# Optimization experiments

Measured on AMD Instinct MI355X. Metric: run time of the kernel, lower is better.

The kernel has to match this reference:

```python
import jax, jax.numpy as jnp
import numpy as np

N_IN = 128 * 128   # flattened stimulus frame
N0 = 4096          # layer 0 neurons
N1 = 1024          # layer 1 neurons
T = 600            # timesteps
MAX_DELAY = 16
DECAY = 0.9
THRESH = 1.0
V_RESET = 0.0


def setup_inputs() -> dict:
    key = jax.random.key(0)
    k1, k2, k3, k4 = jax.random.split(key, 4)
    stim = jax.random.uniform(k1, (128, 128, T), dtype=jnp.float32) * 20.0
    W0 = jax.random.normal(k2, (N0, N_IN), dtype=jnp.float32) * 0.02
    W1 = jax.random.normal(k3, (N1, N0), dtype=jnp.float32) * 0.05
    delays = jax.random.randint(k4, (N1, N0), 0, MAX_DELAY, dtype=jnp.int32)
    return {"stim": stim, "W0": W0, "W1": W1, "delays": delays}


def reference(stim, W0, W1, delays):
    # stim: [H, W, T]; flatten frames -> [T, N_IN]
    t_len = stim.shape[2]
    x = stim.reshape(-1, t_len).T
    jpre = jnp.arange(W0.shape[0])  # presynaptic index per column of W1

    def lif(v, I, dtype):
        v = v * DECAY + I
        s = (v >= THRESH).astype(dtype)
        v = jnp.where(s > 0, V_RESET, v)
        return v, s

    def step(carry, xt):
        v0, v1, buf = carry
        # synapse 0: dense weighted sum of input frame
        I0 = W0 @ xt                                  # [N0]
        v0, s0 = lif(v0, I0, xt.dtype)
        # push newest spikes into circular delay buffer [MAX_DELAY, N0]
        buf = jnp.concatenate([s0[None, :], buf[:-1]], axis=0)
        # synapse 1: per-connection delayed spike gather
        delayed = buf[delays, jpre[None, :]]          # [N1, N0]
        I1 = jnp.sum(W1 * delayed, axis=1)            # [N1]
        v1, s1 = lif(v1, I1, xt.dtype)
        return (v0, v1, buf), (s0, s1)

    init = (
        jnp.zeros((W0.shape[0],), stim.dtype),
        jnp.zeros((W1.shape[0],), stim.dtype),
        jnp.zeros((MAX_DELAY, W0.shape[0]), stim.dtype),
    )
    # loop runs for t in [1, T) as in the original feedforward
    _, (S0, S1) = jax.lax.scan(step, init, x[1:])
    # spike_times layout: [n_neurons, T-1]
    return S0.T, S1.T
```

## Files before the change

kernel.cpp:

```cpp
#include <hip/hip_runtime.h>
#include <stdint.h>
#include <math.h>

#define T_STEPS 599
#define T_RAW   600
#define NIN     16384
#define N0      4096
#define N1      1024
#define S0W     24
#define TAUP    640

typedef double d4 __attribute__((ext_vector_type(4)));

static const size_t OFF_I0T = 0;
static const size_t SZ_I0T  = (size_t)T_STEPS * N0 * 4;
static const size_t OFF_S0B = OFF_I0T + SZ_I0T;
static const size_t SZ_S0B  = (size_t)N0 * S0W * 4;
static const size_t OFF_XT  = OFF_S0B + SZ_S0B;
static const size_t SZ_XT   = (size_t)TAUP * NIN * 4;

__global__ __launch_bounds__(256) void transpose_stim(const float* __restrict__ stim,
                                                      float* __restrict__ Xt) {
    __shared__ float T[64][65];
    const int tau0 = blockIdx.x * 64;
    const int k0   = blockIdx.y * 64;
    const int tid  = threadIdx.x;
    const int kk = tid >> 2;
    const int tb = tid & 3;
#pragma unroll
    for (int q = 0; q < 16; ++q) {
        const int tl = tb + 4 * q;
        const int tg = tau0 + tl;
        float v = 0.0f;
        if (tg <= T_STEPS - 1) v = stim[(size_t)(k0 + kk) * T_RAW + tg + 1];
        T[kk][tl] = v;
    }
    __syncthreads();
    const int tt = tid >> 2;
    const int kq = (tid & 3) * 16;
#pragma unroll
    for (int j = 0; j < 4; ++j) {
        const int kl = kq + 4 * j;
        float4 o;
        o.x = T[kl + 0][tt]; o.y = T[kl + 1][tt];
        o.z = T[kl + 2][tt]; o.w = T[kl + 3][tt];
        *reinterpret_cast<float4*>(&Xt[(size_t)(tau0 + tt) * NIN + k0 + kl]) = o;
    }
}

__global__ __launch_bounds__(256, 5) void gemm_i0_xt(const float* __restrict__ W0,
                                                     const float* __restrict__ Xt,
                                                     float* __restrict__ I0T) {
    __shared__ __align__(16) char smem[31744];
    float* As0 = (float*)(smem);
    float* As1 = (float*)(smem + 4608);
    float* Bt0 = (float*)(smem + 9216);
    float* Bt1 = (float*)(smem + 20480);
    const int tid  = threadIdx.x;
    const int lane = tid & 63;
    const int wid  = tid >> 6;
    const int kbase = 16 * (wid >> 1);
    const int coff  = 32 * (wid & 1);
    const int flat = blockIdx.x;
    const int idx  = (flat & 7) * 160 + (flat >> 3);
    const int n0   = (idx / 10) * 32;
    const int tau0 = (idx % 10) * 64;
    const int r15  = lane & 15;
    const int c    = lane >> 4;

    d4 zero = {0.0, 0.0, 0.0, 0.0};
    const double ap1 = (c == 0) ? 1.0 : 0.0;
    const double bp1 = (c == 0) ? (double)r15 : 0.0;
    d4 pcol = __builtin_amdgcn_mfma_f64_16x16x4f64(ap1, bp1, zero, 0, 0, 0);
    const double ap2 = (c == 0) ? (double)r15 : 0.0;
    const double bp2 = (c == 0) ? 1.0 : 0.0;
    d4 prow = __builtin_amdgcn_mfma_f64_16x16x4f64(ap2, bp2, zero, 0, 0, 0);
    int rowr[4], colr[4];
#pragma unroll
    for (int r = 0; r < 4; ++r) {
        int cc = (int)pcol[r]; cc = cc < 0 ? 0 : (cc > 15 ? 15 : cc);
        int rw = (int)prow[r]; rw = rw < 0 ? 0 : (rw > 15 ? 15 : rw);
        colr[r] = cc; rowr[r] = rw;
    }

    const int ar   = tid >> 3;
    const int ac4  = (tid & 7) * 4;
    const int btau = tid >> 2;
    const int bk8  = (tid & 3) * 8;

    const float* aP  = W0 + (size_t)(n0 + ar) * NIN + ac4;
    const float* xP  = Xt + (size_t)(tau0 + btau) * NIN + bk8;

    float4 aR, bR0, bR1;

#define XLOAD()                                                           \
    aR  = *reinterpret_cast<const float4*>(aP);                           \
    bR0 = *reinterpret_cast<const float4*>(xP);                           \
    bR1 = *reinterpret_cast<const float4*>(xP + 4);                       \
    aP += 32; xP += 32;

#define XSTAGE(AS, BS)                                                    \
    *reinterpret_cast<float4*>(&AS[ar * 36 + ac4]) = aR;                  \
    *reinterpret_cast<float4*>(&BS[btau * 44 + bk8]) = bR0;               \
    *reinterpret_cast<float4*>(&BS[btau * 44 + bk8 + 4]) = bR1;

    d4 c00 = {0,0,0,0}, c01 = {0,0,0,0};
    d4 c10 = {0,0,0,0}, c11 = {0,0,0,0};

#define XMFMA(AS, BS)                                                     \
    {                                                                     \
        __builtin_amdgcn_s_setprio(1);                                    \
        const float4 a0f = *reinterpret_cast<const float4*>(&AS[r15 * 36 + kbase + 4 * c]);        \
        const float4 a1f = *reinterpret_cast<const float4*>(&AS[(16 + r15) * 36 + kbase + 4 * c]); \
        const float4 b0f = *reinterpret_cast<const float4*>(&BS[(coff + r15) * 44 + kbase + 4 * c]);      \
        const float4 b1f = *reinterpret_cast<const float4*>(&BS[(coff + 16 + r15) * 44 + kbase + 4 * c]); \
        c00 = __builtin_amdgcn_mfma_f64_16x16x4f64((double)a0f.x, (double)b0f.x, c00, 0, 0, 0);    \
        c01 = __builtin_amdgcn_mfma_f64_16x16x4f64((double)a0f.x, (double)b1f.x, c01, 0, 0, 0);    \
        c10 = __builtin_amdgcn_mfma_f64_16x16x4f64((double)a1f.x, (double)b0f.x, c10, 0, 0, 0);    \
        c11 = __builtin_amdgcn_mfma_f64_16x16x4f64((double)a1f.x, (double)b1f.x, c11, 0, 0, 0);    \
        c00 = __builtin_amdgcn_mfma_f64_16x16x4f64((double)a0f.y, (double)b0f.y, c00, 0, 0, 0);    \
        c01 = __builtin_amdgcn_mfma_f64_16x16x4f64((double)a0f.y, (double)b1f.y, c01, 0, 0, 0);    \
        c10 = __builtin_amdgcn_mfma_f64_16x16x4f64((double)a1f.y, (double)b0f.y, c10, 0, 0, 0);    \
        c11 = __builtin_amdgcn_mfma_f64_16x16x4f64((double)a1f.y, (double)b1f.y, c11, 0, 0, 0);    \
        c00 = __builtin_amdgcn_mfma_f64_16x16x4f64((double)a0f.z, (double)b0f.z, c00, 0, 0, 0);    \
        c01 = __builtin_amdgcn_mfma_f64_16x16x4f64((double)a0f.z, (double)b1f.z, c01, 0, 0, 0);    \
        c10 = __builtin_amdgcn_mfma_f64_16x16x4f64((double)a1f.z, (double)b0f.z, c10, 0, 0, 0);    \
        c11 = __builtin_amdgcn_mfma_f64_16x16x4f64((double)a1f.z, (double)b1f.z, c11, 0, 0, 0);    \
        c00 = __builtin_amdgcn_mfma_f64_16x16x4f64((double)a0f.w, (double)b0f.w, c00, 0, 0, 0);    \
        c01 = __builtin_amdgcn_mfma_f64_16x16x4f64((double)a0f.w, (double)b1f.w, c01, 0, 0, 0);    \
        c10 = __builtin_amdgcn_mfma_f64_16x16x4f64((double)a1f.w, (double)b0f.w, c10, 0, 0, 0);    \
        c11 = __builtin_amdgcn_mfma_f64_16x16x4f64((double)a1f.w, (double)b1f.w, c11, 0, 0, 0);    \
        __builtin_amdgcn_s_setprio(0);                                    \
    }

    XLOAD();
    for (int chp = 0; chp < 256; ++chp) {
        XSTAGE(As0, Bt0);
        __syncthreads();
        XLOAD();
        XMFMA(As0, Bt0);
        XSTAGE(As1, Bt1);
        __syncthreads();
        if (chp + 1 < 256) { XLOAD(); }
        XMFMA(As1, Bt1);
    }
#undef XLOAD
#undef XSTAGE
#undef XMFMA

    __syncthreads();
    double* Cred = (double*)smem;

#define CRED_OP(OP)                                                       \
    _Pragma("unroll")                                                     \
    for (int r = 0; r < 4; ++r) {                                         \
        const int ro = rowr[r], co = coff + colr[r];                      \
        Cred[(co     ) * 32 + ro     ] OP c00[r];                         \
        Cred[(co + 16) * 32 + ro     ] OP c01[r];                         \
        Cred[(co     ) * 32 + ro + 16] OP c10[r];                         \
        Cred[(co + 16) * 32 + ro + 16] OP c11[r];                         \
    }
    if (wid < 2)  { CRED_OP(=) }
    __syncthreads();
    if (wid >= 2) { CRED_OP(+=) }
    __syncthreads();
#undef CRED_OP

    const int scol = tid >> 2;
    const int srow = (tid & 3) * 8;
    const int tcol = tau0 + scol;
    if (tcol < T_STEPS) {
        const double* cp = &Cred[scol * 32 + srow];
        float4 o0, o1;
        o0.x = (float)cp[0]; o0.y = (float)cp[1]; o0.z = (float)cp[2]; o0.w = (float)cp[3];
        o1.x = (float)cp[4]; o1.y = (float)cp[5]; o1.z = (float)cp[6]; o1.w = (float)cp[7];
        float* op = &I0T[(size_t)tcol * N0 + n0 + srow];
        *reinterpret_cast<float4*>(op)     = o0;
        *reinterpret_cast<float4*>(op + 4) = o1;
    }
}

__global__ __launch_bounds__(256, 5) void gemm_i0_fb(const float* __restrict__ W0,
                                                     const float* __restrict__ stim,
                                                     float* __restrict__ I0T) {
    __shared__ __align__(16) char smem[27904];
    float* As0 = (float*)(smem);
    float* As1 = (float*)(smem + 4736);
    float* Bs0 = (float*)(smem + 9472);
    float* Bs1 = (float*)(smem + 18688);
    const int tid  = threadIdx.x;
    const int lane = tid & 63;
    const int wid  = tid >> 6;
    const int kbase = 16 * (wid >> 1);
    const int coff  = 32 * (wid & 1);
    const int flat = blockIdx.x;
    const int idx  = (flat & 7) * 160 + (flat >> 3);
    const int n0   = (idx / 10) * 32;
    const int tau0 = (idx % 10) * 64;
    const int r15  = lane & 15;
    const int c    = lane >> 4;
    d4 zero = {0.0, 0.0, 0.0, 0.0};
    const double ap1 = (c == 0) ? 1.0 : 0.0;
    const double bp1 = (c == 0) ? (double)r15 : 0.0;
    d4 pcol = __builtin_amdgcn_mfma_f64_16x16x4f64(ap1, bp1, zero, 0, 0, 0);
    const double ap2 = (c == 0) ? (double)r15 : 0.0;
    const double bp2 = (c == 0) ? 1.0 : 0.0;
    d4 prow = __builtin_amdgcn_mfma_f64_16x16x4f64(ap2, bp2, zero, 0, 0, 0);
    int rowr[4], colr[4];
#pragma unroll
    for (int r = 0; r < 4; ++r) {
        int cc = (int)pcol[r]; cc = cc < 0 ? 0 : (cc > 15 ? 15 : cc);
        int rw = (int)prow[r]; rw = rw < 0 ? 0 : (rw > 15 ? 15 : rw);
        colr[r] = cc; rowr[r] = rw;
    }
    const int ar  = tid >> 3;
    const int ac4 = (tid & 7) * 4;
    const int br  = tid >> 4;
    const int bc4 = (tid & 15) * 4;
    const int t0g = tau0 + bc4;
    const bool fastB = (tau0 + 68) <= T_RAW;
    const float* aP  = W0 + (size_t)(n0 + ar) * NIN + ac4;
    const float* bP0 = stim + (size_t)br * T_RAW + t0g;
    const float* bP1 = stim + (size_t)(br + 16) * T_RAW + t0g;
    float4 aR, bRa, bRb;
#define FLOAD()                                                           \
    aR = *reinterpret_cast<const float4*>(aP);                            \
    if (fastB) {                                                          \
        float4 f0 = *reinterpret_cast<const float4*>(bP0);                \
        float  e0 = bP0[4];                                               \
        bRa.x = f0.y; bRa.y = f0.z; bRa.z = f0.w; bRa.w = e0;             \
        float4 f1 = *reinterpret_cast<const float4*>(bP1);                \
        float  e1 = bP1[4];                                               \
        bRb.x = f1.y; bRb.y = f1.z; bRb.z = f1.w; bRb.w = e1;             \
    } else {                                                              \
        bRa.x = (t0g + 0 < T_STEPS) ? bP0[1] : 0.0f;                      \
        bRa.y = (t0g + 1 < T_STEPS) ? bP0[2] : 0.0f;                      \
        bRa.z = (t0g + 2 < T_STEPS) ? bP0[3] : 0.0f;                      \
        bRa.w = (t0g + 3 < T_STEPS) ? bP0[4] : 0.0f;                      \
        bRb.x = (t0g + 0 < T_STEPS) ? bP1[1] : 0.0f;                      \
        bRb.y = (t0g + 1 < T_STEPS) ? bP1[2] : 0.0f;                      \
        bRb.z = (t0g + 2 < T_STEPS) ? bP1[3] : 0.0f;                      \
        bRb.w = (t0g + 3 < T_STEPS) ? bP1[4] : 0.0f;                      \
    }                                                                     \
    aP += 32; bP0 += 32 * T_RAW; bP1 += 32 * T_RAW;
#define FSTAGE(AS, BS)                                                    \
    *reinterpret_cast<float4*>(&AS[ar * 37 + ac4]) = aR;                  \
    *reinterpret_cast<float4*>(&BS[br * 72 + bc4]) = bRa;                 \
    *reinterpret_cast<float4*>(&BS[(br + 16) * 72 + bc4]) = bRb;
#define FKSTEP(AS, BS, KK)                                                \
    {                                                                     \
        const double a0 = (double)AS[r15 * 37 + (KK)];                    \
        const double a1 = (double)AS[(16 + r15) * 37 + (KK)];             \
        const double b0 = (double)BS[(KK) * 72 + coff + r15];             \
        const double b1 = (double)BS[(KK) * 72 + coff + 16 + r15];        \
        c00 = __builtin_amdgcn_mfma_f64_16x16x4f64(a0, b0, c00, 0, 0, 0); \
        c01 = __builtin_amdgcn_mfma_f64_16x16x4f64(a0, b1, c01, 0, 0, 0); \
        c10 = __builtin_amdgcn_mfma_f64_16x16x4f64(a1, b0, c10, 0, 0, 0); \
        c11 = __builtin_amdgcn_mfma_f64_16x16x4f64(a1, b1, c11, 0, 0, 0); \
    }
#define FMFMA(AS, BS)                                                     \
    __builtin_amdgcn_s_setprio(1);                                        \
    FKSTEP(AS, BS, kbase + c);                                            \
    FKSTEP(AS, BS, kbase + 4 + c);                                        \
    FKSTEP(AS, BS, kbase + 8 + c);                                        \
    FKSTEP(AS, BS, kbase + 12 + c);                                       \
    __builtin_amdgcn_s_setprio(0);
    d4 c00 = {0,0,0,0}, c01 = {0,0,0,0};
    d4 c10 = {0,0,0,0}, c11 = {0,0,0,0};
    FLOAD();
    for (int chp = 0; chp < 256; ++chp) {
        FSTAGE(As0, Bs0);
        __syncthreads();
        FLOAD();
        FMFMA(As0, Bs0);
        FSTAGE(As1, Bs1);
        __syncthreads();
        if (chp + 1 < 256) { FLOAD(); }
        FMFMA(As1, Bs1);
    }
#undef FLOAD
#undef FSTAGE
#undef FKSTEP
#undef FMFMA
    __syncthreads();
    double* Cred = (double*)smem;
#define CRED_OP(OP)                                                       \
    _Pragma("unroll")                                                     \
    for (int r = 0; r < 4; ++r) {                                         \
        const int ro = rowr[r], co = coff + colr[r];                      \
        Cred[(co     ) * 32 + ro     ] OP c00[r];                         \
        Cred[(co + 16) * 32 + ro     ] OP c01[r];                         \
        Cred[(co     ) * 32 + ro + 16] OP c10[r];                         \
        Cred[(co + 16) * 32 + ro + 16] OP c11[r];                         \
    }
    if (wid < 2)  { CRED_OP(=) }
    __syncthreads();
    if (wid >= 2) { CRED_OP(+=) }
    __syncthreads();
#undef CRED_OP
    const int scol = tid >> 2;
    const int srow = (tid & 3) * 8;
    const int tcol = tau0 + scol;
    if (tcol < T_STEPS) {
        const double* cp = &Cred[scol * 32 + srow];
        float4 o0, o1;
        o0.x = (float)cp[0]; o0.y = (float)cp[1]; o0.z = (float)cp[2]; o0.w = (float)cp[3];
        o1.x = (float)cp[4]; o1.y = (float)cp[5]; o1.z = (float)cp[6]; o1.w = (float)cp[7];
        float* op = &I0T[(size_t)tcol * N0 + n0 + srow];
        *reinterpret_cast<float4*>(op)     = o0;
        *reinterpret_cast<float4*>(op + 4) = o1;
    }
}

__global__ void lif0(const float* __restrict__ I0T, uint32_t* __restrict__ S0P) {
#pragma clang fp contract(off)
    const int n = blockIdx.x * 64 + threadIdx.x;
    uint32_t* rowp = S0P + n * S0W;
    rowp[0] = 0u;
    rowp[20] = 0u; rowp[21] = 0u; rowp[22] = 0u; rowp[23] = 0u;
    float v = 0.0f;
    uint32_t word = 0;
    int t = 0;
    for (; t + 8 <= T_STEPS; t += 8) {
        float I[8];
#pragma unroll
        for (int u = 0; u < 8; ++u) I[u] = I0T[(size_t)(t + u) * N0 + n];
#pragma unroll
        for (int u = 0; u < 8; ++u) {
            const int tt = t + u;
            float a = v * 0.9f;
            v = a + I[u];
            if (v >= 1.0f) { word |= (1u << (tt & 31)); v = 0.0f; }
            if ((tt & 31) == 31) { rowp[1 + (tt >> 5)] = word; word = 0; }
        }
    }
    for (; t < T_STEPS; ++t) {
        float I = I0T[(size_t)t * N0 + n];
        float a = v * 0.9f;
        v = a + I;
        if (v >= 1.0f) { word |= (1u << (t & 31)); v = 0.0f; }
        if ((t & 31) == 31) { rowp[1 + (t >> 5)] = word; word = 0; }
    }
    rowp[1 + (T_STEPS >> 5)] = word;
}

__global__ __launch_bounds__(128) void gather_lif1(const float* __restrict__ W1,
                                                   const int* __restrict__ delays,
                                                   const uint32_t* __restrict__ S0P,
                                                   float* __restrict__ out) {
#pragma clang fp contract(off)
    __shared__ double  wl[N0];
    __shared__ uint8_t dl[N0];
    __shared__ float   i1row[T_RAW];
    const int j   = blockIdx.x;
    const int tid = threadIdx.x;
    for (int q = tid; q < N0 / 4; q += 128) {
        const float4 w4 = *reinterpret_cast<const float4*>(&W1[(size_t)j * N0 + 4 * q]);
        wl[4 * q + 0] = (double)w4.x; wl[4 * q + 1] = (double)w4.y;
        wl[4 * q + 2] = (double)w4.z; wl[4 * q + 3] = (double)w4.w;
        const int4 dv = *reinterpret_cast<const int4*>(&delays[(size_t)j * N0 + 4 * q]);
        dl[4 * q + 0] = (uint8_t)dv.x; dl[4 * q + 1] = (uint8_t)dv.y;
        dl[4 * q + 2] = (uint8_t)dv.z; dl[4 * q + 3] = (uint8_t)dv.w;
    }
    __syncthreads();
    const int t5 = 5 * tid;
    double a0 = 0.0, a1 = 0.0, a2 = 0.0, a3 = 0.0, a4 = 0.0;
    const uint32_t* rp0 = S0P + 1;
#pragma unroll 2
    for (int i = 0; i < N0; ++i) {
        const int s0  = t5 - (int)dl[i];
        const double w = wl[i];
        const int widx = (s0 >> 5);
        const int sh   = s0 & 31;
        const uint32_t lo = rp0[widx];
        const uint32_t hi = rp0[widx + 1];
        const uint32_t w5 = (uint32_t)(((((uint64_t)hi) << 32) | lo) >> sh);
        a0 = fma((double)( w5       & 1u), w, a0);
        a1 = fma((double)((w5 >> 1) & 1u), w, a1);
        a2 = fma((double)((w5 >> 2) & 1u), w, a2);
        a3 = fma((double)((w5 >> 3) & 1u), w, a3);
        a4 = fma((double)((w5 >> 4) & 1u), w, a4);
        rp0 += S0W;
    }
    if (tid < 120) {
        i1row[t5 + 0] = (float)a0;
        i1row[t5 + 1] = (float)a1;
        i1row[t5 + 2] = (float)a2;
        i1row[t5 + 3] = (float)a3;
        i1row[t5 + 4] = (float)a4;
    }
    __syncthreads();
    if (tid == 0) {
        float* o = out + (size_t)N0 * T_STEPS + (size_t)j * T_STEPS;
        float v = 0.0f;
        for (int t = 0; t < T_STEPS; ++t) {
            float a = v * 0.9f;
            v = a + i1row[t];
            float s = 0.0f;
            if (v >= 1.0f) { s = 1.0f; v = 0.0f; }
            o[t] = s;
        }
    }
}

__global__ void expand_out(const uint32_t* __restrict__ S0P,
                           float* __restrict__ out) {
    const int t = blockIdx.x * 256 + threadIdx.x;
    if (t >= T_STEPS) return;
    const int row = blockIdx.y;
    uint32_t b = (S0P[row * S0W + 1 + (t >> 5)] >> (t & 31)) & 1u;
    out[(size_t)row * T_STEPS + t] = (float)b;
}

extern "C" void kernel_launch(void* const* d_in, const int* in_sizes, int n_in,
                              void* d_out, int out_size, void* d_ws, size_t ws_size,
                              hipStream_t stream) {
    const float* stim   = (const float*)d_in[0];
    const float* W0     = (const float*)d_in[1];
    const float* W1     = (const float*)d_in[2];
    const int*   delays = (const int*)d_in[3];

    char* ws = (char*)d_ws;
    float*    I0T  = (float*)(ws + OFF_I0T);
    uint32_t* S0b  = (uint32_t*)(ws + OFF_S0B);
    float*    Xt   = (float*)(ws + OFF_XT);
    float*    out  = (float*)d_out;

    if (ws_size >= OFF_XT + SZ_XT) {
        hipLaunchKernelGGL(transpose_stim, dim3(10, 256), dim3(256), 0, stream, stim, Xt);
        hipLaunchKernelGGL(gemm_i0_xt,     dim3(1280),    dim3(256), 0, stream, W0, Xt, I0T);
    } else {
        hipLaunchKernelGGL(gemm_i0_fb,     dim3(1280),    dim3(256), 0, stream, W0, stim, I0T);
    }
    hipLaunchKernelGGL(lif0,        dim3(64),    dim3(64),  0, stream, I0T, S0b);
    hipLaunchKernelGGL(gather_lif1, dim3(1024),  dim3(128), 0, stream, W1, delays, S0b, out);
    hipLaunchKernelGGL(expand_out,  dim3(3, N0), dim3(256), 0, stream, S0b, out);
}
```

Baseline: 2.205 ms.

## Fuse S0 output expansion into lif0 and split gather across two halves

The layer-0 LIF kernel now writes float spikes to the output directly, going through a shared-memory transpose tile, so the separate expand_out kernel is removed. The delayed-gather kernel is split so each block handles half of the presynaptic neurons, which doubles the grid to 2048 blocks. Partial sums are written in double to workspace that reuses the I0T region, and a new combine kernel adds the two halves and runs the layer-1 LIF scan. The aim is more parallelism in the gather stage and one less launch, at the cost of an extra launch and a round trip through the double partials. Splitting the sum into two halves also changes the order of the double-precision accumulation.

New measurement: 1.861 ms. 15.6% less time.

```diff
diff --git a/kernel.cpp b/kernel.cpp
--- a/kernel.cpp
+++ b/kernel.cpp
@@ -312,62 +312,82 @@
     }
 }
 
-__global__ void lif0(const float* __restrict__ I0T, uint32_t* __restrict__ S0P) {
+__global__ void lif0x(const float* __restrict__ I0T, uint32_t* __restrict__ S0P,
+                      float* __restrict__ out) {
 #pragma clang fp contract(off)
-    const int n = blockIdx.x * 64 + threadIdx.x;
+    __shared__ float tile[64][65];
+    const int l  = threadIdx.x;
+    const int n0 = blockIdx.x * 64;
+    const int n  = n0 + l;
     uint32_t* rowp = S0P + n * S0W;
     rowp[0] = 0u;
     rowp[20] = 0u; rowp[21] = 0u; rowp[22] = 0u; rowp[23] = 0u;
     float v = 0.0f;
     uint32_t word = 0;
-    int t = 0;
-    for (; t + 8 <= T_STEPS; t += 8) {
-        float I[8];
-#pragma unroll
-        for (int u = 0; u < 8; ++u) I[u] = I0T[(size_t)(t + u) * N0 + n];
-#pragma unroll
-        for (int u = 0; u < 8; ++u) {
-            const int tt = t + u;
+    for (int b = 0; b < 10; ++b) {
+        const int tbase = b * 64;
+        const int tcnt  = (tbase + 64 <= T_STEPS) ? 64 : (T_STEPS - tbase);
+        int u = 0;
+        for (; u + 8 <= tcnt; u += 8) {
+            float I[8];
+#pragma unroll
+            for (int k = 0; k < 8; ++k) I[k] = I0T[(size_t)(tbase + u + k) * N0 + n];
+#pragma unroll
+            for (int k = 0; k < 8; ++k) {
+                const int tt = tbase + u + k;
+                float a = v * 0.9f;
+                v = a + I[k];
+                float s = 0.0f;
+                if (v >= 1.0f) { word |= (1u << (tt & 31)); v = 0.0f; s = 1.0f; }
+                tile[l][u + k] = s;
+                if ((tt & 31) == 31) { rowp[1 + (tt >> 5)] = word; word = 0; }
+            }
+        }
+        for (; u < tcnt; ++u) {
+            const int tt = tbase + u;
+            float I = I0T[(size_t)tt * N0 + n];
             float a = v * 0.9f;
-            v = a + I[u];
-            if (v >= 1.0f) { word |= (1u << (tt & 31)); v = 0.0f; }
+            v = a + I;
+            float s = 0.0f;
+            if (v >= 1.0f) { word |= (1u << (tt & 31)); v = 0.0f; s = 1.0f; }
+            tile[l][u] = s;
             if ((tt & 31) == 31) { rowp[1 + (tt >> 5)] = word; word = 0; }
         }
-    }
-    for (; t < T_STEPS; ++t) {
-        float I = I0T[(size_t)t * N0 + n];
-        float a = v * 0.9f;
-        v = a + I;
-        if (v >= 1.0f) { word |= (1u << (t & 31)); v = 0.0f; }
-        if ((t & 31) == 31) { rowp[1 + (t >> 5)] = word; word = 0; }
+        __syncthreads();
+        if (l < tcnt) {
+#pragma unroll 8
+            for (int r = 0; r < 64; ++r)
+                out[(size_t)(n0 + r) * T_STEPS + tbase + l] = tile[r][l];
+        }
+        __syncthreads();
     }
     rowp[1 + (T_STEPS >> 5)] = word;
 }
 
-__global__ __launch_bounds__(128) void gather_lif1(const float* __restrict__ W1,
+__global__ __launch_bounds__(128) void gather_half(const float* __restrict__ W1,
                                                    const int* __restrict__ delays,
                                                    const uint32_t* __restrict__ S0P,
-                                                   float* __restrict__ out) {
-#pragma clang fp contract(off)
-    __shared__ double  wl[N0];
-    __shared__ uint8_t dl[N0];
-    __shared__ float   i1row[T_RAW];
-    const int j   = blockIdx.x;
-    const int tid = threadIdx.x;
-    for (int q = tid; q < N0 / 4; q += 128) {
-        const float4 w4 = *reinterpret_cast<const float4*>(&W1[(size_t)j * N0 + 4 * q]);
+                                                   double* __restrict__ part) {
+    __shared__ double  wl[2048];
+    __shared__ uint8_t dl[2048];
+    const int bid  = blockIdx.x;
+    const int j    = bid >> 1;
+    const int ibase = (bid & 1) * 2048;
+    const int tid  = threadIdx.x;
+    for (int q = tid; q < 2048 / 4; q += 128) {
+        const float4 w4 = *reinterpret_cast<const float4*>(&W1[(size_t)j * N0 + ibase + 4 * q]);
         wl[4 * q + 0] = (double)w4.x; wl[4 * q + 1] = (double)w4.y;
         wl[4 * q + 2] = (double)w4.z; wl[4 * q + 3] = (double)w4.w;
-        const int4 dv = *reinterpret_cast<const int4*>(&delays[(size_t)j * N0 + 4 * q]);
+        const int4 dv = *reinterpret_cast<const int4*>(&delays[(size_t)j * N0 + ibase + 4 * q]);
         dl[4 * q + 0] = (uint8_t)dv.x; dl[4 * q + 1] = (uint8_t)dv.y;
         dl[4 * q + 2] = (uint8_t)dv.z; dl[4 * q + 3] = (uint8_t)dv.w;
     }
     __syncthreads();
     const int t5 = 5 * tid;
     double a0 = 0.0, a1 = 0.0, a2 = 0.0, a3 = 0.0, a4 = 0.0;
-    const uint32_t* rp0 = S0P + 1;
+    const uint32_t* rp0 = S0P + (size_t)ibase * S0W + 1;
 #pragma unroll 2
-    for (int i = 0; i < N0; ++i) {
+    for (int i = 0; i < 2048; ++i) {
         const int s0  = t5 - (int)dl[i];
         const double w = wl[i];
         const int widx = (s0 >> 5);
@@ -383,14 +403,24 @@
         rp0 += S0W;
     }
     if (tid < 120) {
-        i1row[t5 + 0] = (float)a0;
-        i1row[t5 + 1] = (float)a1;
-        i1row[t5 + 2] = (float)a2;
-        i1row[t5 + 3] = (float)a3;
-        i1row[t5 + 4] = (float)a4;
-    }
-    __syncthreads();
-    if (tid == 0) {
+        double* op = part + (size_t)bid * T_STEPS + t5;
+        op[0] = a0; op[1] = a1; op[2] = a2; op[3] = a3;
+        if (t5 + 4 < T_STEPS) op[4] = a4;
+    }
+}
+
+__global__ __launch_bounds__(64) void combine_lif1(const double* __restrict__ part,
+                                                   float* __restrict__ out) {
+#pragma clang fp contract(off)
+    __shared__ float i1row[T_RAW];
+    const int j = blockIdx.x;
+    const int l = threadIdx.x;
+    const double* p0 = part + (size_t)(2 * j)     * T_STEPS;
+    const double* p1 = part + (size_t)(2 * j + 1) * T_STEPS;
+    for (int t = l; t < T_STEPS; t += 64)
+        i1row[t] = (float)(p0[t] + p1[t]);
+    __syncthreads();
+    if (l == 0) {
         float* o = out + (size_t)N0 * T_STEPS + (size_t)j * T_STEPS;
         float v = 0.0f;
         for (int t = 0; t < T_STEPS; ++t) {
@@ -403,15 +433,6 @@
     }
 }
 
-__global__ void expand_out(const uint32_t* __restrict__ S0P,
-                           float* __restrict__ out) {
-    const int t = blockIdx.x * 256 + threadIdx.x;
-    if (t >= T_STEPS) return;
-    const int row = blockIdx.y;
-    uint32_t b = (S0P[row * S0W + 1 + (t >> 5)] >> (t & 31)) & 1u;
-    out[(size_t)row * T_STEPS + t] = (float)b;
-}
-
 extern "C" void kernel_launch(void* const* d_in, const int* in_sizes, int n_in,
                               void* d_out, int out_size, void* d_ws, size_t ws_size,
                               hipStream_t stream) {
@@ -422,6 +443,7 @@
 
     char* ws = (char*)d_ws;
     float*    I0T  = (float*)(ws + OFF_I0T);
+    double*   part = (double*)(ws + OFF_I0T);
     uint32_t* S0b  = (uint32_t*)(ws + OFF_S0B);
     float*    Xt   = (float*)(ws + OFF_XT);
     float*    out  = (float*)d_out;
@@ -432,7 +454,7 @@
     } else {
         hipLaunchKernelGGL(gemm_i0_fb,     dim3(1280),    dim3(256), 0, stream, W0, stim, I0T);
     }
-    hipLaunchKernelGGL(lif0,        dim3(64),    dim3(64),  0, stream, I0T, S0b);
-    hipLaunchKernelGGL(gather_lif1, dim3(1024),  dim3(128), 0, stream, W1, delays, S0b, out);
-    hipLaunchKernelGGL(expand_out,  dim3(3, N0), dim3(256), 0, stream, S0b, out);
-}
+    hipLaunchKernelGGL(lif0x,        dim3(64),   dim3(64),  0, stream, I0T, S0b, out);
+    hipLaunchKernelGGL(gather_half,  dim3(2048), dim3(128), 0, stream, W1, delays, S0b, part);
+    hipLaunchKernelGGL(combine_lif1, dim3(1024), dim3(64),  0, stream, part, out);
+}
```
